# Optimization experiments

Measured on AMD Instinct MI355X. Metric: run time of the kernel, lower is better.

Reference implementation:

```python
import math
import jax, jax.numpy as jnp
import numpy as np

HEADS = 8


def setup_inputs() -> dict:
    key = jax.random.key(0)
    k1, k2, k3 = jax.random.split(key, 3)
    b, n, a, dim = 1, 256, 256, 512
    init_scale = 0.02
    x = jax.random.normal(k1, (b, n, a, dim), dtype=jnp.float32)
    w_qkv = jax.random.normal(k2, (dim, 3 * dim), dtype=jnp.float32) * init_scale
    b_qkv = jnp.zeros((3 * dim,), dtype=jnp.float32)
    w_proj = jax.random.normal(k3, (dim, dim), dtype=jnp.float32) * init_scale
    b_proj = jnp.zeros((dim,), dtype=jnp.float32)
    return {"x": x, "w_qkv": w_qkv, "b_qkv": b_qkv, "w_proj": w_proj, "b_proj": b_proj}


def reference(x, w_qkv, b_qkv, w_proj, b_proj):
    b, n, a, dim = x.shape
    dh = dim // HEADS
    scale = 1.0 / math.sqrt(math.sqrt(dh))
    qkv = jnp.einsum('bnad,de->bnae', x, w_qkv) + b_qkv  # [b,n,a,3*dim]
    qkv = qkv.reshape(b, n, a, HEADS, 3 * dh)
    q, k, v = jnp.split(qkv, 3, axis=-1)  # each [b,n,a,h,dh]
    # scores over the 'a' axis, independent per (b, n, head)
    sim = jnp.einsum('bnihd,bnjhd->bnhij', q * scale, k * scale)
    attn = jax.nn.softmax(sim, axis=-1)
    out = jnp.einsum('bnhij,bnjhd->bnihd', attn, v).reshape(b, n, a, dim)
    return jnp.einsum('bnad,de->bnae', out, w_proj) + b_proj
```

## Files before the change

### kernel.cpp

```cpp
#include <hip/hip_runtime.h>

typedef unsigned short u16;
typedef unsigned int u32;
typedef __bf16 bf16x8 __attribute__((ext_vector_type(8)));
typedef float f32x4 __attribute__((ext_vector_type(4)));

__device__ __forceinline__ u16 f2b(float f) {
  u32 u = __builtin_bit_cast(u32, f);
  u32 r = (u + 0x7fffu + ((u >> 16) & 1u)) >> 16;
  return (u16)r;
}
__device__ __forceinline__ bf16x8 ld_frag(const u16* p) {
  uint4 v = *(const uint4*)p;
  return __builtin_bit_cast(bf16x8, v);
}
__device__ __forceinline__ void async_lds16(const u16* g, u16* lds) {
  __builtin_amdgcn_global_load_lds(
      (const __attribute__((address_space(1))) void*)g,
      (__attribute__((address_space(3))) void*)lds, 16, 0, 0);
}
__device__ __forceinline__ void wait_lds() { __builtin_amdgcn_s_waitcnt(0xc07f); }

__global__ __launch_bounds__(256) void convert_f32_bf16(const float* __restrict__ in,
                                                        u16* __restrict__ out) {
  long i = ((long)blockIdx.x * 256 + threadIdx.x) * 8;
  float4 a = *(const float4*)(in + i);
  float4 b = *(const float4*)(in + i + 4);
  union { uint4 v; u16 e[8]; } u;
  u.e[0] = f2b(a.x); u.e[1] = f2b(a.y); u.e[2] = f2b(a.z); u.e[3] = f2b(a.w);
  u.e[4] = f2b(b.x); u.e[5] = f2b(b.y); u.e[6] = f2b(b.z); u.e[7] = f2b(b.w);
  *(uint4*)(out + i) = u.v;
}

__global__ __launch_bounds__(256) void transpose_w(const float* __restrict__ W,
                                                   u16* __restrict__ Wt,
                                                   int K, int N) {
  __shared__ alignas(16) u16 T[64][80];
  const int n0 = blockIdx.x * 64, k0 = blockIdx.y * 64;
  const int t = threadIdx.x;
  {
    int kk = t >> 3, c = t & 7;
#pragma unroll
    for (int rr = 0; rr < 2; ++rr) {
      int kr = kk + rr * 32;
      const float* src = W + (long)(k0 + kr) * N + n0 + c * 8;
      float4 a = *(const float4*)src;
      float4 b = *(const float4*)(src + 4);
      u16* dst = &T[kr][c * 8];
      dst[0] = f2b(a.x); dst[1] = f2b(a.y); dst[2] = f2b(a.z); dst[3] = f2b(a.w);
      dst[4] = f2b(b.x); dst[5] = f2b(b.y); dst[6] = f2b(b.z); dst[7] = f2b(b.w);
    }
  }
  __syncthreads();
  {
    int nn = t >> 3, kc = t & 7;
#pragma unroll
    for (int rr = 0; rr < 2; ++rr) {
      int nr = nn + rr * 32;
      union { uint4 v; u16 e[8]; } u;
#pragma unroll
      for (int i = 0; i < 8; ++i) u.e[i] = T[kc * 8 + i][nr];
      *(uint4*)(Wt + (long)(n0 + nr) * K + k0 + kc * 8) = u.v;
    }
  }
}

template <bool OUT_F32>
__global__ __launch_bounds__(256, 2) void gemm_pipe(const u16* __restrict__ A,
                                                    const u16* __restrict__ Bt,
                                                    const float* __restrict__ bias,
                                                    void* __restrict__ Cv,
                                                    int M, int N, int K) {
  __shared__ alignas(16) u16 lds[3 * 12288];
  const int tid = threadIdx.x;
  const int lane = tid & 63, wave = tid >> 6;
  const int quad = lane >> 4, ln = lane & 15;
  const int wm = wave >> 1, wn = wave & 1;

  const int nwg = gridDim.x;
  const int bid = blockIdx.x;
  const int wg = (bid & 7) * (nwg >> 3) + (bid >> 3);
  const int ntn = N >> 7;
  const int tn = wg % ntn, tm = wg / ntn;
  const long m0 = (long)tm * 256;
  const long n0 = (long)tn * 128;

  const int srow = lane >> 2;
  const int swz = ((lane & 3) ^ (srow & 3)) * 8;
  const u16* gA[4];
  const u16* gB[2];
#pragma unroll
  for (int u = 0; u < 4; ++u) gA[u] = A + (long)(m0 + u * 64 + wave * 16 + srow) * K + swz;
#pragma unroll
  for (int v = 0; v < 2; ++v) gB[v] = Bt + (long)(n0 + v * 64 + wave * 16 + srow) * K + swz;

  const int KT = K >> 5;

  auto stageP1 = [&](int t) {
    if (t >= KT) return;
    u16* s = &lds[(t % 3) * 12288 + wave * 512];
    long ko = (long)t * 32;
    async_lds16(gA[0] + ko, s);
    async_lds16(gA[1] + ko, s + 2048);
    async_lds16(gA[2] + ko, s + 4096);
  };
  auto stageP2 = [&](int t) {
    if (t >= KT) return;
    u16* s = &lds[(t % 3) * 12288 + wave * 512];
    long ko = (long)t * 32;
    async_lds16(gA[3] + ko, s + 6144);
    async_lds16(gB[0] + ko, s + 8192);
    async_lds16(gB[1] + ko, s + 8192 + 2048);
  };

  const int cswz = (quad ^ (ln & 3)) * 8;
  auto ldA = [&](int t, int mt) {
    int row = wm * 128 + mt * 16 + ln;
    return ld_frag(&lds[(t % 3) * 12288 + row * 32 + cswz]);
  };
  auto ldB = [&](int t, int nt) {
    int row = wn * 64 + nt * 16 + ln;
    return ld_frag(&lds[(t % 3) * 12288 + 8192 + row * 32 + cswz]);
  };

  f32x4 zero = {0.f, 0.f, 0.f, 0.f};
  f32x4 acc[8][4];
#pragma unroll
  for (int i = 0; i < 8; ++i)
#pragma unroll
    for (int j = 0; j < 4; ++j) acc[i][j] = zero;

  stageP1(0); stageP2(0);
  stageP1(1); stageP2(1);
  __builtin_amdgcn_s_waitcnt(0x0f76);
  __builtin_amdgcn_s_barrier();

  bf16x8 bf[4], alo[4], ahi[4];
#pragma unroll
  for (int nt = 0; nt < 4; ++nt) bf[nt] = ldB(0, nt);
#pragma unroll
  for (int mt = 0; mt < 4; ++mt) alo[mt] = ldA(0, mt);

  for (int t = 0; t < KT; ++t) {
#pragma unroll
    for (int mt = 0; mt < 4; ++mt) ahi[mt] = ldA(t, mt + 4);
    stageP1(t + 2);
#pragma unroll
    for (int mt = 0; mt < 4; ++mt)
#pragma unroll
      for (int nt = 0; nt < 4; ++nt)
        acc[mt][nt] = __builtin_amdgcn_mfma_f32_16x16x32_bf16(alo[mt], bf[nt], acc[mt][nt], 0, 0, 0);
    if (t + 1 < KT) {
      if (t + 2 < KT) __builtin_amdgcn_s_waitcnt(0x0f73);
      else            __builtin_amdgcn_s_waitcnt(0x0f70);
      wait_lds();
      __builtin_amdgcn_s_barrier();
      bf16x8 nbf[4], nalo[4];
#pragma unroll
      for (int nt = 0; nt < 4; ++nt) nbf[nt] = ldB(t + 1, nt);
#pragma unroll
      for (int mt = 0; mt < 4; ++mt) nalo[mt] = ldA(t + 1, mt);
      stageP2(t + 2);
#pragma unroll
      for (int mt = 0; mt < 4; ++mt)
#pragma unroll
        for (int nt = 0; nt < 4; ++nt)
          acc[mt + 4][nt] = __builtin_amdgcn_mfma_f32_16x16x32_bf16(ahi[mt], bf[nt], acc[mt + 4][nt], 0, 0, 0);
#pragma unroll
      for (int nt = 0; nt < 4; ++nt) bf[nt] = nbf[nt];
#pragma unroll
      for (int mt = 0; mt < 4; ++mt) alo[mt] = nalo[mt];
    } else {
#pragma unroll
      for (int mt = 0; mt < 4; ++mt)
#pragma unroll
        for (int nt = 0; nt < 4; ++nt)
          acc[mt + 4][nt] = __builtin_amdgcn_mfma_f32_16x16x32_bf16(ahi[mt], bf[nt], acc[mt + 4][nt], 0, 0, 0);
    }
  }

  __syncthreads();

  if (OUT_F32) {
#pragma unroll
    for (int nt = 0; nt < 4; ++nt) {
      long coln = n0 + wn * 64 + nt * 16 + ln;
      float bv = bias[coln];
#pragma unroll
      for (int mt = 0; mt < 8; ++mt) {
        long rowb = m0 + wm * 128 + mt * 16 + quad * 4;
#pragma unroll
        for (int r = 0; r < 4; ++r)
          ((float*)Cv)[(rowb + r) * N + coln] = acc[mt][nt][r] + bv;
      }
    }
  } else {
    u16* patch = &lds[wave * 2176];
    float bv[4];
#pragma unroll
    for (int nt = 0; nt < 4; ++nt) bv[nt] = bias[n0 + wn * 64 + nt * 16 + ln];
#pragma unroll
    for (int mt = 0; mt < 8; ++mt) {
#pragma unroll
      for (int nt = 0; nt < 4; ++nt)
#pragma unroll
        for (int r = 0; r < 4; ++r)
          patch[(quad * 4 + r) * 136 + nt * 16 + ln] = f2b(acc[mt][nt][r] + bv[nt]);
      wait_lds();
#pragma unroll
      for (int it = 0; it < 2; ++it) {
        int cid = it * 64 + lane;
        int row = cid >> 3, ch = cid & 7;
        uint4 v = *(const uint4*)&patch[row * 136 + ch * 8];
        *(uint4*)&((u16*)Cv)[(m0 + wm * 128 + mt * 16 + row) * (long)N + n0 + wn * 64 + ch * 8] = v;
      }
      wait_lds();
    }
  }
}

__global__ __launch_bounds__(256, 2) void attn_fused(const u16* __restrict__ qkv,
                                                     u16* __restrict__ out) {
  __shared__ alignas(16) u16 Ks[256 * 64];
  __shared__ alignas(16) u16 Vt[64 * 256];
  const int h = blockIdx.x;
  const long n = blockIdx.y;
  const int tid = threadIdx.x;
  const int lane = tid & 63, wave = tid >> 6;
  const int quad = lane >> 4, ln = lane & 15;
  const u16* base = qkv + (n * 256) * 1536 + h * 192;

  auto stageK = [&]() {
    int c = tid & 7, jb = tid >> 3;
#pragma unroll
    for (int rr = 0; rr < 8; ++rr) {
      int j = jb + rr * 32;
      uint4 v = *(const uint4*)(base + (long)j * 1536 + 64 + c * 8);
      *(uint4*)&Ks[j * 64 + ((c ^ (j & 7)) * 8)] = v;
    }
  };
  stageK();
  {
    int p = tid & 7, jb = tid >> 3;
#pragma unroll
    for (int rr = 0; rr < 8; ++rr) {
      int j = jb + rr * 32;
      union { uint4 v; u16 e[8]; } u;
      u.v = *(const uint4*)(base + (long)j * 1536 + 128 + p * 8);
      int cj = j >> 3, jl = j & 7;
#pragma unroll
      for (int i = 0; i < 8; ++i) {
        int d = p * 8 + i;
        int key = (p ^ i) & 7;
        Vt[d * 256 + ((cj ^ key) * 8) + jl] = u.e[i];
      }
    }
  }
  __syncthreads();

  u16* Pw = &Ks[wave * 2176];
  f32x4 zero = {0.f, 0.f, 0.f, 0.f};

  for (int s = 0; s < 2; ++s) {
    const int row0 = wave * 64 + s * 32;
    bf16x8 qa[2][2];
#pragma unroll
    for (int mt = 0; mt < 2; ++mt)
#pragma unroll
      for (int kc = 0; kc < 2; ++kc)
        qa[mt][kc] = ld_frag(base + (long)(row0 + mt * 16 + ln) * 1536 + kc * 32 + quad * 8);

    f32x4 sacc[2][16];
#pragma unroll
    for (int mt = 0; mt < 2; ++mt)
#pragma unroll
      for (int jt = 0; jt < 16; ++jt) sacc[mt][jt] = zero;

#pragma unroll
    for (int jt = 0; jt < 16; ++jt) {
#pragma unroll
      for (int kc = 0; kc < 2; ++kc) {
        bf16x8 kb = ld_frag(&Ks[(jt * 16 + ln) * 64 + (((kc * 4 + quad) ^ (ln & 7)) * 8)]);
        sacc[0][jt] = __builtin_amdgcn_mfma_f32_16x16x32_bf16(qa[0][kc], kb, sacc[0][jt], 0, 0, 0);
        sacc[1][jt] = __builtin_amdgcn_mfma_f32_16x16x32_bf16(qa[1][kc], kb, sacc[1][jt], 0, 0, 0);
      }
    }
    __syncthreads();

#pragma unroll
    for (int mt = 0; mt < 2; ++mt) {
      float linv[4];
#pragma unroll
      for (int r = 0; r < 4; ++r) {
        float mx = -3.0e38f;
#pragma unroll
        for (int jt = 0; jt < 16; ++jt) mx = fmaxf(mx, sacc[mt][jt][r]);
        mx = fmaxf(mx, __shfl_xor(mx, 1));
        mx = fmaxf(mx, __shfl_xor(mx, 2));
        mx = fmaxf(mx, __shfl_xor(mx, 4));
        mx = fmaxf(mx, __shfl_xor(mx, 8));
        float l = 0.f;
#pragma unroll
        for (int jt = 0; jt < 16; ++jt) {
          float p = __expf((sacc[mt][jt][r] - mx) * 0.125f);
          sacc[mt][jt][r] = p;
          l += p;
        }
        l += __shfl_xor(l, 1);
        l += __shfl_xor(l, 2);
        l += __shfl_xor(l, 4);
        l += __shfl_xor(l, 8);
        linv[r] = 1.0f / l;
      }

      f32x4 oacc[4];
#pragma unroll
      for (int dt = 0; dt < 4; ++dt) oacc[dt] = zero;
#pragma unroll
      for (int jh = 0; jh < 2; ++jh) {
#pragma unroll
        for (int jl = 0; jl < 8; ++jl) {
          int jt = jh * 8 + jl;
#pragma unroll
          for (int r = 0; r < 4; ++r)
            Pw[(quad * 4 + r) * 136 + jl * 16 + ln] = f2b(sacc[mt][jt][r]);
        }
        wait_lds();
#pragma unroll
        for (int jcl = 0; jcl < 4; ++jcl) {
          bf16x8 pa = ld_frag(&Pw[ln * 136 + jcl * 32 + quad * 8]);
          int cjb = (jh * 4 + jcl) * 4 + quad;
#pragma unroll
          for (int dt = 0; dt < 4; ++dt) {
            int d = dt * 16 + ln;
            int key = ((d >> 3) ^ d) & 7;
            bf16x8 vb = ld_frag(&Vt[d * 256 + ((cjb ^ key) * 8)]);
            oacc[dt] = __builtin_amdgcn_mfma_f32_16x16x32_bf16(pa, vb, oacc[dt], 0, 0, 0);
          }
        }
      }
#pragma unroll
      for (int dt = 0; dt < 4; ++dt)
#pragma unroll
        for (int r = 0; r < 4; ++r)
          Pw[(quad * 4 + r) * 136 + dt * 16 + ln] = f2b(oacc[dt][r] * linv[r]);
      wait_lds();
#pragma unroll
      for (int it = 0; it < 2; ++it) {
        int cid = it * 64 + lane;
        int row = cid >> 3, ch = cid & 7;
        uint4 v = *(const uint4*)&Pw[row * 136 + ch * 8];
        *(uint4*)&out[(n * 256 + row0 + mt * 16 + row) * 512 + h * 64 + ch * 8] = v;
      }
    }
    __syncthreads();
    if (s == 0) {
      stageK();
      __syncthreads();
    }
  }
}

extern "C" void kernel_launch(void* const* d_in, const int* in_sizes, int n_in,
                              void* d_out, int out_size, void* d_ws, size_t ws_size,
                              hipStream_t stream) {
  const float* x      = (const float*)d_in[0];
  const float* w_qkv  = (const float*)d_in[1];
  const float* b_qkv  = (const float*)d_in[2];
  const float* w_proj = (const float*)d_in[3];
  const float* b_proj = (const float*)d_in[4];
  float* out = (float*)d_out;

  char* ws = (char*)d_ws;
  u16* xb   = (u16*)ws;
  u16* qkv  = (u16*)(ws + 67108864L);
  u16* attn = (u16*)(ws + 67108864L + 201326592L);
  u16* Wt1  = (u16*)(ws + 67108864L + 201326592L + 67108864L);
  u16* Wt2  = Wt1 + 1536 * 512;

  convert_f32_bf16<<<16384, 256, 0, stream>>>(x, xb);
  transpose_w<<<dim3(24, 8), 256, 0, stream>>>(w_qkv, Wt1, 512, 1536);
  transpose_w<<<dim3(8, 8), 256, 0, stream>>>(w_proj, Wt2, 512, 512);
  gemm_pipe<false><<<dim3(12 * 256), 256, 0, stream>>>(xb, Wt1, b_qkv, qkv, 65536, 1536, 512);
  attn_fused<<<dim3(8, 256), 256, 0, stream>>>(qkv, attn);
  gemm_pipe<true><<<dim3(4 * 256), 256, 0, stream>>>(attn, Wt2, b_proj, out, 65536, 512, 512);
}
```

Before: 593.2 us.

## Enlarge GEMM tile to 256x256 with 8 waves and interleaved staging

```diff
diff --git a/kernel.cpp b/kernel.cpp
--- a/kernel.cpp
+++ b/kernel.cpp
@@ -66,61 +66,53 @@
 }
 
 template <bool OUT_F32>
-__global__ __launch_bounds__(256, 2) void gemm_pipe(const u16* __restrict__ A,
+__global__ __launch_bounds__(512, 2) void gemm_pipe(const u16* __restrict__ A,
                                                     const u16* __restrict__ Bt,
                                                     const float* __restrict__ bias,
                                                     void* __restrict__ Cv,
                                                     int M, int N, int K) {
-  __shared__ alignas(16) u16 lds[3 * 12288];
+  __shared__ alignas(16) u16 lds[3 * 16384];
   const int tid = threadIdx.x;
   const int lane = tid & 63, wave = tid >> 6;
   const int quad = lane >> 4, ln = lane & 15;
-  const int wm = wave >> 1, wn = wave & 1;
+  const int wm = wave >> 2, wn = wave & 3;
 
   const int nwg = gridDim.x;
   const int bid = blockIdx.x;
   const int wg = (bid & 7) * (nwg >> 3) + (bid >> 3);
-  const int ntn = N >> 7;
+  const int ntn = N >> 8;
   const int tn = wg % ntn, tm = wg / ntn;
   const long m0 = (long)tm * 256;
-  const long n0 = (long)tn * 128;
-
-  const int srow = lane >> 2;
-  const int swz = ((lane & 3) ^ (srow & 3)) * 8;
-  const u16* gA[4];
+  const long n0 = (long)tn * 256;
+
+  const int srow = wave * 16 + (lane >> 2);
+  const int gsw = ((lane & 3) ^ ((lane >> 3) & 3)) * 8;
+  const u16* gA[2];
   const u16* gB[2];
 #pragma unroll
-  for (int u = 0; u < 4; ++u) gA[u] = A + (long)(m0 + u * 64 + wave * 16 + srow) * K + swz;
-#pragma unroll
-  for (int v = 0; v < 2; ++v) gB[v] = Bt + (long)(n0 + v * 64 + wave * 16 + srow) * K + swz;
+  for (int u = 0; u < 2; ++u) gA[u] = A + (long)(m0 + u * 128 + srow) * K + gsw;
+#pragma unroll
+  for (int u = 0; u < 2; ++u) gB[u] = Bt + (long)(n0 + u * 128 + srow) * K + gsw;
 
   const int KT = K >> 5;
 
-  auto stageP1 = [&](int t) {
-    if (t >= KT) return;
-    u16* s = &lds[(t % 3) * 12288 + wave * 512];
-    long ko = (long)t * 32;
-    async_lds16(gA[0] + ko, s);
-    async_lds16(gA[1] + ko, s + 2048);
-    async_lds16(gA[2] + ko, s + 4096);
-  };
-  auto stageP2 = [&](int t) {
-    if (t >= KT) return;
-    u16* s = &lds[(t % 3) * 12288 + wave * 512];
-    long ko = (long)t * 32;
-    async_lds16(gA[3] + ko, s + 6144);
-    async_lds16(gB[0] + ko, s + 8192);
-    async_lds16(gB[1] + ko, s + 8192 + 2048);
-  };
-
-  const int cswz = (quad ^ (ln & 3)) * 8;
+  auto stageA = [&](int t, int u) {
+    u16* s = &lds[(t % 3) * 16384 + u * 4096 + wave * 512];
+    async_lds16(gA[u] + (long)t * 32, s);
+  };
+  auto stageB = [&](int t, int u) {
+    u16* s = &lds[(t % 3) * 16384 + 8192 + u * 4096 + wave * 512];
+    async_lds16(gB[u] + (long)t * 32, s);
+  };
+
+  const int cpos = (quad ^ ((ln >> 1) & 3)) * 8;
   auto ldA = [&](int t, int mt) {
     int row = wm * 128 + mt * 16 + ln;
-    return ld_frag(&lds[(t % 3) * 12288 + row * 32 + cswz]);
+    return ld_frag(&lds[(t % 3) * 16384 + row * 32 + cpos]);
   };
   auto ldB = [&](int t, int nt) {
     int row = wn * 64 + nt * 16 + ln;
-    return ld_frag(&lds[(t % 3) * 12288 + 8192 + row * 32 + cswz]);
+    return ld_frag(&lds[(t % 3) * 16384 + 8192 + row * 32 + cpos]);
   };
 
   f32x4 zero = {0.f, 0.f, 0.f, 0.f};
@@ -130,53 +122,54 @@
 #pragma unroll
     for (int j = 0; j < 4; ++j) acc[i][j] = zero;
 
-  stageP1(0); stageP2(0);
-  stageP1(1); stageP2(1);
-  __builtin_amdgcn_s_waitcnt(0x0f76);
+  stageA(0, 0); stageA(0, 1); stageB(0, 0); stageB(0, 1);
+  stageA(1, 0); stageA(1, 1); stageB(1, 0); stageB(1, 1);
+  __builtin_amdgcn_s_waitcnt(0x0f74);
   __builtin_amdgcn_s_barrier();
 
-  bf16x8 bf[4], alo[4], ahi[4];
-#pragma unroll
-  for (int nt = 0; nt < 4; ++nt) bf[nt] = ldB(0, nt);
-#pragma unroll
-  for (int mt = 0; mt < 4; ++mt) alo[mt] = ldA(0, mt);
-
   for (int t = 0; t < KT; ++t) {
-#pragma unroll
-    for (int mt = 0; mt < 4; ++mt) ahi[mt] = ldA(t, mt + 4);
-    stageP1(t + 2);
+    bf16x8 Alo[4], Ahi[4], Bl[2], Bh[2];
+#pragma unroll
+    for (int mt = 0; mt < 4; ++mt) Alo[mt] = ldA(t, mt);
+    Bl[0] = ldB(t, 0); Bl[1] = ldB(t, 1);
+    if (t + 2 < KT) stageA(t + 2, 0);
+    __builtin_amdgcn_s_setprio(1);
 #pragma unroll
     for (int mt = 0; mt < 4; ++mt)
 #pragma unroll
-      for (int nt = 0; nt < 4; ++nt)
-        acc[mt][nt] = __builtin_amdgcn_mfma_f32_16x16x32_bf16(alo[mt], bf[nt], acc[mt][nt], 0, 0, 0);
-    if (t + 1 < KT) {
-      if (t + 2 < KT) __builtin_amdgcn_s_waitcnt(0x0f73);
-      else            __builtin_amdgcn_s_waitcnt(0x0f70);
-      wait_lds();
-      __builtin_amdgcn_s_barrier();
-      bf16x8 nbf[4], nalo[4];
-#pragma unroll
-      for (int nt = 0; nt < 4; ++nt) nbf[nt] = ldB(t + 1, nt);
-#pragma unroll
-      for (int mt = 0; mt < 4; ++mt) nalo[mt] = ldA(t + 1, mt);
-      stageP2(t + 2);
-#pragma unroll
-      for (int mt = 0; mt < 4; ++mt)
-#pragma unroll
-        for (int nt = 0; nt < 4; ++nt)
-          acc[mt + 4][nt] = __builtin_amdgcn_mfma_f32_16x16x32_bf16(ahi[mt], bf[nt], acc[mt + 4][nt], 0, 0, 0);
-#pragma unroll
-      for (int nt = 0; nt < 4; ++nt) bf[nt] = nbf[nt];
-#pragma unroll
-      for (int mt = 0; mt < 4; ++mt) alo[mt] = nalo[mt];
-    } else {
-#pragma unroll
-      for (int mt = 0; mt < 4; ++mt)
-#pragma unroll
-        for (int nt = 0; nt < 4; ++nt)
-          acc[mt + 4][nt] = __builtin_amdgcn_mfma_f32_16x16x32_bf16(ahi[mt], bf[nt], acc[mt + 4][nt], 0, 0, 0);
-    }
+      for (int nt = 0; nt < 2; ++nt)
+        acc[mt][nt] = __builtin_amdgcn_mfma_f32_16x16x32_bf16(Alo[mt], Bl[nt], acc[mt][nt], 0, 0, 0);
+    __builtin_amdgcn_s_setprio(0);
+#pragma unroll
+    for (int mt = 0; mt < 4; ++mt) Ahi[mt] = ldA(t, mt + 4);
+    if (t + 2 < KT) stageA(t + 2, 1);
+    __builtin_amdgcn_s_setprio(1);
+#pragma unroll
+    for (int mt = 0; mt < 4; ++mt)
+#pragma unroll
+      for (int nt = 0; nt < 2; ++nt)
+        acc[mt + 4][nt] = __builtin_amdgcn_mfma_f32_16x16x32_bf16(Ahi[mt], Bl[nt], acc[mt + 4][nt], 0, 0, 0);
+    __builtin_amdgcn_s_setprio(0);
+    Bh[0] = ldB(t, 2); Bh[1] = ldB(t, 3);
+    if (t + 2 < KT) stageB(t + 2, 0);
+    __builtin_amdgcn_s_setprio(1);
+#pragma unroll
+    for (int mt = 0; mt < 4; ++mt)
+#pragma unroll
+      for (int nt = 0; nt < 2; ++nt)
+        acc[mt][nt + 2] = __builtin_amdgcn_mfma_f32_16x16x32_bf16(Alo[mt], Bh[nt], acc[mt][nt + 2], 0, 0, 0);
+    __builtin_amdgcn_s_setprio(0);
+    if (t + 2 < KT) stageB(t + 2, 1);
+    __builtin_amdgcn_s_setprio(1);
+#pragma unroll
+    for (int mt = 0; mt < 4; ++mt)
+#pragma unroll
+      for (int nt = 0; nt < 2; ++nt)
+        acc[mt + 4][nt + 2] = __builtin_amdgcn_mfma_f32_16x16x32_bf16(Ahi[mt], Bh[nt], acc[mt + 4][nt + 2], 0, 0, 0);
+    __builtin_amdgcn_s_setprio(0);
+    if (t + 2 < KT)      __builtin_amdgcn_s_waitcnt(0x0f74);
+    else if (t + 1 < KT) __builtin_amdgcn_s_waitcnt(0x0f70);
+    __builtin_amdgcn_s_barrier();
   }
 
   __syncthreads();
@@ -381,7 +374,7 @@
   convert_f32_bf16<<<16384, 256, 0, stream>>>(x, xb);
   transpose_w<<<dim3(24, 8), 256, 0, stream>>>(w_qkv, Wt1, 512, 1536);
   transpose_w<<<dim3(8, 8), 256, 0, stream>>>(w_proj, Wt2, 512, 512);
-  gemm_pipe<false><<<dim3(12 * 256), 256, 0, stream>>>(xb, Wt1, b_qkv, qkv, 65536, 1536, 512);
+  gemm_pipe<false><<<dim3(6 * 256), 512, 0, stream>>>(xb, Wt1, b_qkv, qkv, 65536, 1536, 512);
   attn_fused<<<dim3(8, 256), 256, 0, stream>>>(qkv, attn);
-  gemm_pipe<true><<<dim3(4 * 256), 256, 0, stream>>>(attn, Wt2, b_proj, out, 65536, 512, 512);
-}
+  gemm_pipe<true><<<dim3(2 * 256), 512, 0, stream>>>(attn, Wt2, b_proj, out, 65536, 512, 512);
+}
```

Result: faster. 566.6 us (-4.5%).
